# Optimization experiments

Measured on AMD Instinct MI355X. Metric: run time of the kernel, lower is better.

## Reference

```python
import jax, jax.numpy as jnp
import numpy as np

N = 50000      # nodes
E = 800000     # original edges (no self loops)
D = 128        # in_channels == hidden_channels
NEG = 0.2      # leaky_relu negative slope
LAMB = 0.1


def setup_inputs() -> dict:
    key = jax.random.key(0)
    ks = jax.random.split(key, 10)
    s = 0.05
    x = jax.random.normal(ks[0], (N, D), jnp.float32)
    src = jax.random.randint(ks[1], (E,), 0, N)
    off = jax.random.randint(ks[2], (E,), 1, N)
    dst = (src + off) % N  # guaranteed non-self-loop
    loop = jnp.arange(N)
    # add_remaining_self_loops appends the N self loops at the end
    edge_index = jnp.stack([jnp.concatenate([src, loop]),
                            jnp.concatenate([dst, loop])]).astype(jnp.int32)
    return {
        "x": x,
        "edge_index": edge_index,
        "W_gcn": jax.random.normal(ks[3], (D, D), jnp.float32) * s,
        "b_gcn": jnp.zeros((D,), jnp.float32),
        "W_key": jax.random.normal(ks[4], (D, 1), jnp.float32) * s,
        "b_key": jnp.zeros((1,), jnp.float32),
        "W_query": jax.random.normal(ks[5], (D, 1), jnp.float32) * s,
        "b_query": jnp.zeros((1,), jnp.float32),
        "W_rel": jax.random.normal(ks[6], (D, 1), jnp.float32) * s,
        "b_rel": jnp.zeros((1,), jnp.float32),
        "W_root": jax.random.normal(ks[7], (D, 1), jnp.float32) * s,
    }


def _segment_softmax(s, idx, n):
    # numerically stable softmax grouped by idx (every segment nonempty: self loops)
    m = jax.ops.segment_max(s, idx, num_segments=n)
    e = jnp.exp(s - m[idx])
    z = jax.ops.segment_sum(e, idx, num_segments=n)
    return e / z[idx]


def reference(x, edge_index, W_gcn, b_gcn, W_key, b_key, W_query, b_query,
              W_rel, b_rel, W_root):
    n = x.shape[0]
    row, col = edge_index[0], edge_index[1]  # source, target

    # --- GCNConv transform_neighbor (self loops already present) ---
    ew = jnp.ones(row.shape, x.dtype)
    deg = jax.ops.segment_sum(ew, col, num_segments=n)
    dinv = jnp.where(deg > 0, jax.lax.rsqrt(deg), 0.0)
    norm = dinv[row] * dinv[col]                      # [Etot]
    xw = x @ W_gcn                                    # [N, D]
    x_transform = jax.ops.segment_sum(norm[:, None] * xw[row], col,
                                      num_segments=n) + b_gcn  # [N, D]

    x_neighbor = x_transform[col]                     # [Etot, D]

    # key branch: linear -> leaky_relu -> segment softmax over row -> scatter add
    key_s = jax.nn.leaky_relu((x_neighbor @ W_key + b_key)[:, 0], NEG)
    key_s = _segment_softmax(key_s, row, n)[:, None]
    x_reweight_key = jax.ops.segment_sum(x_neighbor * key_s, row, num_segments=n)

    # query branch
    qry_s = jax.nn.leaky_relu((x_neighbor @ W_query + b_query)[:, 0], NEG)
    qry_s = _segment_softmax(qry_s, row, n)[:, None]
    x_reweight_query = jax.ops.segment_sum(x_neighbor * qry_s, row, num_segments=n)

    ker_error = jnp.sum(jnp.abs(x_reweight_key[row] - x_transform[row]), axis=1)
    query_error = jnp.sum(jnp.abs(x_reweight_query[row] - x_transform[col]), axis=1)
    red_score = (ker_error - query_error).at[-n:].set(0.0)  # zero self-loop edges
    score_sum = jax.ops.segment_sum(red_score, row, num_segments=n)

    # --- GraphConv gnn_score: lin_rel(sum_j x_j) + lin_root(x), then sigmoid ---
    agg = jax.ops.segment_sum(x[row], col, num_segments=n)
    fitness = jax.nn.sigmoid((agg @ W_rel + b_rel + x @ W_root)[:, 0])

    return fitness - LAMB * score_sum
```

## Files before the change

### kernel.cpp

```cpp
#include <hip/hip_runtime.h>
#include <math.h>

#define D 128
#define CAP 64
#define NEG 0.2f
#define LAMB 0.1f
#define PB 512
#define SCAP 416
#define NB2 98

__device__ inline float waveReduceSum(float v) {
    #pragma unroll
    for (int m = 32; m; m >>= 1) v += __shfl_xor(v, m);
    return v;
}
__device__ inline float waveReduceMax(float v) {
    #pragma unroll
    for (int m = 32; m; m >>= 1) v = fmaxf(v, __shfl_xor(v, m));
    return v;
}
__device__ inline float blockReduceSum128(float v, float* lds) {
    v = waveReduceSum(v);
    int w = threadIdx.x >> 6;
    if ((threadIdx.x & 63) == 0) lds[w] = v;
    __syncthreads();
    float r = lds[0] + lds[1];
    __syncthreads();
    return r;
}

__device__ inline float bf2f(unsigned short u) {
    union { unsigned int i; float f; } v;
    v.i = ((unsigned int)u) << 16;
    return v.f;
}
__device__ inline float bfLo(unsigned int u) {
    union { unsigned int i; float f; } v;
    v.i = u << 16;
    return v.f;
}
__device__ inline float bfHi(unsigned int u) {
    union { unsigned int i; float f; } v;
    v.i = u & 0xffff0000u;
    return v.f;
}
__device__ inline unsigned short f2bf(float f) {
    union { float f; unsigned int i; } v;
    v.f = f;
    unsigned int b = v.i;
    b += 0x7fff + ((b >> 16) & 1);
    return (unsigned short)(b >> 16);
}

__global__ __launch_bounds__(256) void k_part(
    const int* __restrict__ ei, int etot, int eorig, int q,
    unsigned int* __restrict__ recs, unsigned short* __restrict__ scnt) {
    __shared__ unsigned int bins[16][SCAP];
    __shared__ int bcnt[16];
    const int b = blockIdx.x;
    const int tid = threadIdx.x;
    if (tid < 16) bcnt[tid] = 0;
    __syncthreads();
    const int e0 = (int)((long long)b * eorig / PB);
    const int e1 = (int)((long long)(b + 1) * eorig / PB);
    for (int e = e0 + tid; e < e1; e += 256) {
        int r = ei[e];
        int c = ei[etot + e];
        int gc = c / q;
        int s1 = atomicAdd(&bcnt[gc], 1);
        if (s1 < SCAP) bins[gc][s1] = ((unsigned int)c << 16) | (unsigned int)r;
        int gr = 8 + r / q;
        int s2 = atomicAdd(&bcnt[gr], 1);
        if (s2 < SCAP) bins[gr][s2] = ((unsigned int)r << 16) | (unsigned int)c;
    }
    __syncthreads();
    for (int bk = 0; bk < 16; bk++) {
        int m = min(bcnt[bk], SCAP);
        unsigned int* dst = recs + ((size_t)bk * PB + b) * SCAP;
        for (int i = tid; i < m; i += 256) dst[i] = bins[bk][i];
        if (tid == 0) scnt[bk * PB + b] = (unsigned short)m;
    }
}

__global__ __launch_bounds__(256) void k_partB(
    const unsigned int* __restrict__ recs,
    const unsigned short* __restrict__ scnt, int q,
    unsigned int* __restrict__ recs2, unsigned short* __restrict__ scnt2) {
    const int dirg = blockIdx.x >> 6;
    const int chunk = blockIdx.x & 63;
    const int lo = (dirg & 7) * q;
    __shared__ unsigned int bins[100][64];
    __shared__ int bcnt[100];
    __shared__ int mseg[8];
    const int tid = threadIdx.x;
    for (int i = tid; i < 100; i += 256) bcnt[i] = 0;
    if (tid < 8) mseg[tid] = scnt[dirg * PB + chunk * 8 + tid];
    __syncthreads();
    for (int i = tid; i < 8 * SCAP; i += 256) {
        int seg = i / SCAP, off = i - seg * SCAP;
        if (off < mseg[seg]) {
            unsigned int rec =
                recs[((size_t)dirg * PB + chunk * 8 + seg) * SCAP + off];
            int bk = (int)((rec >> 16) - lo) >> 6;
            if (bk < 100) {
                int s = atomicAdd(&bcnt[bk], 1);
                if (s < 64) bins[bk][s] = rec;
            }
        }
    }
    __syncthreads();
    for (int i = tid; i < NB2 * 64; i += 256) {
        int bk = i >> 6, slot = i & 63;
        int m = min(bcnt[bk], 64);
        if (slot < m)
            recs2[(((size_t)dirg * NB2 + bk) * 64 + chunk) * 64 + slot] =
                bins[bk][slot];
        if (slot == 0)
            scnt2[((size_t)dirg * NB2 + bk) * 64 + chunk] = (unsigned short)m;
    }
}

__global__ __launch_bounds__(256) void k_bld(
    const unsigned int* __restrict__ recs2,
    const unsigned short* __restrict__ scnt2, int q, int n,
    int* __restrict__ cnt_col, int* __restrict__ cnt_row,
    unsigned short* __restrict__ lst_col,
    unsigned short* __restrict__ lst_row) {
    const int dirg = blockIdx.x / NB2;
    const int bk = blockIdx.x - dirg * NB2;
    const int g = dirg & 7;
    const int dir = dirg >> 3;
    const int base = g * q + bk * 64;
    const int hi = min(n, g * q + q);
    const int nb64 = min(64, hi - base);
    if (nb64 <= 0) return;
    __shared__ unsigned short stage[64][CAP];
    __shared__ int scnt3[64];
    __shared__ int mseg[64];
    const int tid = threadIdx.x;
    if (tid < 64) {
        scnt3[tid] = 1;
        stage[tid][0] = (unsigned short)(base + tid);
        mseg[tid] = scnt2[((size_t)dirg * NB2 + bk) * 64 + tid];
    }
    __syncthreads();
    for (int i = tid; i < 64 * 64; i += 256) {
        int seg = i >> 6, slot = i & 63;
        if (slot < mseg[seg]) {
            unsigned int rec =
                recs2[(((size_t)dirg * NB2 + bk) * 64 + seg) * 64 + slot];
            int local = (int)(rec >> 16) - base;
            int s = atomicAdd(&scnt3[local], 1);
            if (s < CAP) stage[local][s] = (unsigned short)(rec & 0xffffu);
        }
    }
    __syncthreads();
    int* cnt = dir ? cnt_row : cnt_col;
    unsigned short* lst = dir ? lst_row : lst_col;
    const int lane = tid & 63;
    const int jo = tid >> 6;
    for (int j0 = 0; j0 < 64; j0 += 4) {
        int j = j0 + jo;
        if (j < nb64) {
            int dg = min(scnt3[j], CAP);
            if (lane < dg) lst[(size_t)(base + j) * CAP + lane] = stage[j][lane];
            if (lane == 0) cnt[base + j] = scnt3[j];
        }
    }
}

__global__ __launch_bounds__(128) void k_gemm(
    const float* __restrict__ x, const float* __restrict__ W,
    const float* __restrict__ Wrel, const float* __restrict__ Wroot,
    unsigned short* __restrict__ xwb, float* __restrict__ xr_rel,
    float* __restrict__ xroot, int n) {
    __shared__ float xs[16][D];
    const int nb = blockIdx.x * 16;
    const int tid = threadIdx.x;
    #pragma unroll
    for (int k = 0; k < 16; k++) {
        int i = nb + k;
        xs[k][tid] = (i < n) ? x[(size_t)i * D + tid] : 0.f;
    }
    __syncthreads();
    float acc[16];
    #pragma unroll
    for (int k = 0; k < 16; k++) acc[k] = 0.f;
    #pragma unroll 4
    for (int d = 0; d < D; d++) {
        float w = W[d * D + tid];
        #pragma unroll
        for (int k = 0; k < 16; k++) acc[k] += xs[k][d] * w;
    }
    #pragma unroll
    for (int k = 0; k < 16; k++) {
        int i = nb + k;
        if (i < n) xwb[(size_t)i * D + tid] = f2bf(acc[k]);
    }
    const int j = tid >> 3;
    const int s = tid & 7;
    float pr = 0.f, po = 0.f;
    #pragma unroll
    for (int e = 0; e < 16; e++) {
        float xv = xs[j][s * 16 + e];
        pr += xv * Wrel[s * 16 + e];
        po += xv * Wroot[s * 16 + e];
    }
    #pragma unroll
    for (int m = 1; m < 8; m <<= 1) {
        pr += __shfl_xor(pr, m);
        po += __shfl_xor(po, m);
    }
    if (s == 0 && nb + j < n) { xr_rel[nb + j] = pr; xroot[nb + j] = po; }
}

__global__ void k_pack(const int* __restrict__ cnt_col,
                       const float* __restrict__ xr_rel,
                       float2* __restrict__ nd, int n) {
    int i = blockIdx.x * blockDim.x + threadIdx.x;
    if (i < n) nd[i] = make_float2(rsqrtf((float)cnt_col[i]), xr_rel[i]);
}

__global__ __launch_bounds__(128) void k_xt(
    const unsigned short* __restrict__ xwb,
    const int* __restrict__ cnt_col, const unsigned short* __restrict__ lst_col,
    const float2* __restrict__ nd, const float* __restrict__ b_gcn,
    const float* __restrict__ Wkey, const float* __restrict__ bkey,
    const float* __restrict__ Wq, const float* __restrict__ bq,
    float* __restrict__ agg_s, unsigned short* __restrict__ xtb,
    float2* __restrict__ lkq, int n) {
    const int c = blockIdx.x;
    const int tid = threadIdx.x;
    const int g = tid >> 5;
    const int l = tid & 31;
    __shared__ int rs[CAP];
    __shared__ float ns[CAP];
    __shared__ float axr[CAP];
    __shared__ float part[4][D];
    __shared__ float red[2];
    int deg = min(cnt_col[c], CAP);
    float dc = nd[c].x;
    if (tid < deg) {
        int rr = lst_col[(size_t)c * CAP + tid];
        rs[tid] = rr;
        float2 t = nd[rr];
        ns[tid] = t.x * dc;
        axr[tid] = t.y;
    }
    __syncthreads();
    if (tid < 64) {
        float av = (tid < deg) ? axr[tid] : 0.f;
        av = waveReduceSum(av);
        if (tid == 0) agg_s[c] = av;
    }
    float4 acc = make_float4(0.f, 0.f, 0.f, 0.f);
#define XSLOT(kk) do {                                                        \
        int k = g + (kk) * 4;                                                 \
        if (k < deg) {                                                        \
            const ushort4 u =                                                 \
                *(const ushort4*)(xwb + (size_t)rs[k] * D + l * 4);           \
            float w = ns[k];                                                  \
            acc.x += w * bf2f(u.x); acc.y += w * bf2f(u.y);                   \
            acc.z += w * bf2f(u.z); acc.w += w * bf2f(u.w);                   \
        }                                                                     \
    } while (0)
    XSLOT(0); XSLOT(1); XSLOT(2); XSLOT(3);
    if (deg > 16) { XSLOT(4); XSLOT(5); }
    if (deg > 24) { XSLOT(6); XSLOT(7); }
    for (int k = g + 32; k < deg; k += 4) {
        const ushort4 u = *(const ushort4*)(xwb + (size_t)rs[k] * D + l * 4);
        float w = ns[k];
        acc.x += w * bf2f(u.x); acc.y += w * bf2f(u.y);
        acc.z += w * bf2f(u.z); acc.w += w * bf2f(u.w);
    }
    *(float4*)(&part[g][l * 4]) = acc;
    __syncthreads();
    float fin = part[0][tid] + part[1][tid] + part[2][tid] + part[3][tid]
                + b_gcn[tid];
    xtb[(size_t)c * D + tid] = f2bf(fin);
    float sk = blockReduceSum128(fin * Wkey[tid], red);
    float sq = blockReduceSum128(fin * Wq[tid], red);
    if (tid == 0) {
        float vk = sk + bkey[0];
        float vq = sq + bq[0];
        lkq[c] = make_float2(vk > 0.f ? vk : NEG * vk,
                             vq > 0.f ? vq : NEG * vq);
    }
}

__global__ __launch_bounds__(128) void k_fused(
    const unsigned short* __restrict__ xtb,
    const int* __restrict__ cnt_row, const unsigned short* __restrict__ lst_row,
    const float2* __restrict__ lkq,
    const float* __restrict__ agg_s, const float* __restrict__ xroot,
    const float* __restrict__ brel, float* __restrict__ out, int n) {
    const int r = blockIdx.x;
    const int tid = threadIdx.x;
    const int g = tid >> 5;
    const int l = tid & 31;
    __shared__ int cs[CAP];
    __shared__ float al[CAP], be[CAP];
    __shared__ float p1[4][D], p2[4][D];
    __shared__ float xrq_row[D];
    __shared__ float red[2];
    int deg = min(cnt_row[r], CAP);
    float xtr = bf2f(xtb[(size_t)r * D + tid]);
    if (tid < deg) {
        int c = lst_row[(size_t)r * CAP + tid];
        cs[tid] = c;
        float2 t = lkq[c];
        al[tid] = t.x;
        be[tid] = t.y;
    }
    __syncthreads();
    uint2 vr[8];
#define LSLOT(kk) do {                                                        \
        int k_ = g + (kk) * 4;                                                \
        vr[kk] = make_uint2(0u, 0u);                                          \
        if (k_ < deg)                                                         \
            vr[kk] = *(const uint2*)(xtb + (size_t)cs[k_] * D + l * 4);       \
    } while (0)
    LSLOT(0); LSLOT(1); LSLOT(2); LSLOT(3);
    if (deg > 16) { LSLOT(4); LSLOT(5); }
    if (deg > 24) { LSLOT(6); LSLOT(7); }
    if (tid < 64) {
        float vk = (tid < deg) ? al[tid] : -3.4e38f;
        float vq = (tid < deg) ? be[tid] : -3.4e38f;
        float mk = waveReduceMax(vk);
        float mq = waveReduceMax(vq);
        float ek = (tid < deg) ? __expf(al[tid] - mk) : 0.f;
        float eq = (tid < deg) ? __expf(be[tid] - mq) : 0.f;
        float zk = waveReduceSum(ek);
        float zq = waveReduceSum(eq);
        if (tid < deg) { al[tid] = ek / zk; be[tid] = eq / zq; }
    }
    __syncthreads();
    float4 xrk = make_float4(0.f, 0.f, 0.f, 0.f);
    float4 xrq = make_float4(0.f, 0.f, 0.f, 0.f);
#define GSLOT(kk) do {                                                        \
        int k_ = g + (kk) * 4;                                                \
        float a_ = 0.f, b_ = 0.f;                                             \
        if (k_ < deg) { a_ = al[k_]; b_ = be[k_]; }                           \
        float v0 = bfLo(vr[kk].x), v1 = bfHi(vr[kk].x);                       \
        float v2 = bfLo(vr[kk].y), v3 = bfHi(vr[kk].y);                       \
        xrk.x += a_ * v0; xrk.y += a_ * v1;                                   \
        xrk.z += a_ * v2; xrk.w += a_ * v3;                                   \
        xrq.x += b_ * v0; xrq.y += b_ * v1;                                   \
        xrq.z += b_ * v2; xrq.w += b_ * v3;                                   \
    } while (0)
    GSLOT(0); GSLOT(1); GSLOT(2); GSLOT(3);
    if (deg > 16) { GSLOT(4); GSLOT(5); }
    if (deg > 24) { GSLOT(6); GSLOT(7); }
    for (int k = g + 32; k < deg; k += 4) {
        const ushort4 u = *(const ushort4*)(xtb + (size_t)cs[k] * D + l * 4);
        float a = al[k], b = be[k];
        xrk.x += a * bf2f(u.x); xrk.y += a * bf2f(u.y);
        xrk.z += a * bf2f(u.z); xrk.w += a * bf2f(u.w);
        xrq.x += b * bf2f(u.x); xrq.y += b * bf2f(u.y);
        xrq.z += b * bf2f(u.z); xrq.w += b * bf2f(u.w);
    }
    *(float4*)(&p1[g][l * 4]) = xrk;
    *(float4*)(&p2[g][l * 4]) = xrq;
    __syncthreads();
    float xrk_c = p1[0][tid] + p1[1][tid] + p1[2][tid] + p1[3][tid];
    float xrq_c = p2[0][tid] + p2[1][tid] + p2[2][tid] + p2[3][tid];
    xrq_row[tid] = xrq_c;
    float KE = blockReduceSum128(fabsf(xrk_c - xtr), red);
    const float4 q4 = *(const float4*)(&xrq_row[l * 4]);
    float sp = 0.f;
#define QSLOT(kk) do {                                                        \
        int k_ = g + (kk) * 4;                                                \
        if (k_ < deg && cs[k_] != r) {                                        \
            sp += fabsf(q4.x - bfLo(vr[kk].x)) + fabsf(q4.y - bfHi(vr[kk].x)) \
                + fabsf(q4.z - bfLo(vr[kk].y)) + fabsf(q4.w - bfHi(vr[kk].y));\
        }                                                                     \
    } while (0)
    QSLOT(0); QSLOT(1); QSLOT(2); QSLOT(3);
    if (deg > 16) { QSLOT(4); QSLOT(5); }
    if (deg > 24) { QSLOT(6); QSLOT(7); }
    for (int k = g + 32; k < deg; k += 4) {
        if (cs[k] != r) {
            const ushort4 u = *(const ushort4*)(xtb + (size_t)cs[k] * D + l * 4);
            sp += fabsf(q4.x - bf2f(u.x)) + fabsf(q4.y - bf2f(u.y)) +
                  fabsf(q4.z - bf2f(u.z)) + fabsf(q4.w - bf2f(u.w));
        }
    }
    float SQE = blockReduceSum128(sp, red);
    if (tid == 0) {
        float score = (float)(deg - 1) * KE - SQE;
        float z = agg_s[r] + brel[0] + xroot[r];
        float f = 1.f / (1.f + __expf(-z));
        out[r] = f - LAMB * score;
    }
}

extern "C" void kernel_launch(void* const* d_in, const int* in_sizes, int n_in,
                              void* d_out, int out_size, void* d_ws, size_t ws_size,
                              hipStream_t stream) {
    const float* x    = (const float*)d_in[0];
    const int*   ei   = (const int*)d_in[1];
    const float* Wg   = (const float*)d_in[2];
    const float* bg   = (const float*)d_in[3];
    const float* Wk   = (const float*)d_in[4];
    const float* bk   = (const float*)d_in[5];
    const float* Wq   = (const float*)d_in[6];
    const float* bq   = (const float*)d_in[7];
    const float* Wr   = (const float*)d_in[8];
    const float* br   = (const float*)d_in[9];
    const float* Wo   = (const float*)d_in[10];

    const int n = in_sizes[0] / D;
    const int etot = in_sizes[1] / 2;
    const int eorig = etot - n;
    const int q = (n + 7) / 8;

    char* ws = (char*)d_ws;
    size_t off = 0;
    auto alloc = [&](size_t bytes) -> void* {
        void* p = ws + off;
        off += (bytes + 255) & ~(size_t)255;
        return p;
    };
    unsigned short* xwb = (unsigned short*)alloc((size_t)n * D * 2);
    unsigned short* xtb = (unsigned short*)alloc((size_t)n * D * 2);
    size_t recsA_bytes = (size_t)16 * PB * SCAP * 4;
    size_t lst_bytes   = (size_t)n * CAP * 2 * 2;
    char* unionA = (char*)alloc(recsA_bytes > lst_bytes ? recsA_bytes
                                                        : lst_bytes);
    unsigned int*   recsA   = (unsigned int*)unionA;
    unsigned short* lst_col = (unsigned short*)unionA;
    unsigned short* lst_row = (unsigned short*)(unionA + (size_t)n * CAP * 2);
    unsigned int*   recs2 = (unsigned int*)alloc((size_t)16 * NB2 * 64 * 64 * 4);
    unsigned short* scnt  = (unsigned short*)alloc((size_t)16 * PB * 2);
    unsigned short* scnt2 = (unsigned short*)alloc((size_t)16 * NB2 * 64 * 2);
    int*    cnt_col = (int*)alloc((size_t)n * 4);
    int*    cnt_row = (int*)alloc((size_t)n * 4);
    float*  agg_s   = (float*)alloc((size_t)n * 4);
    float2* lkq     = (float2*)alloc((size_t)n * 8);
    float2* nd      = (float2*)alloc((size_t)n * 8);
    float*  xr_rel  = (float*)alloc((size_t)n * 4);
    float*  xroot   = (float*)alloc((size_t)n * 4);

    k_part<<<PB, 256, 0, stream>>>(ei, etot, eorig, q, recsA, scnt);
    k_partB<<<16 * 64, 256, 0, stream>>>(recsA, scnt, q, recs2, scnt2);
    k_bld<<<16 * NB2, 256, 0, stream>>>(recs2, scnt2, q, n,
                                        cnt_col, cnt_row, lst_col, lst_row);
    k_gemm<<<(n + 15) / 16, 128, 0, stream>>>(x, Wg, Wr, Wo, xwb, xr_rel,
                                              xroot, n);
    k_pack<<<(n + 255) / 256, 256, 0, stream>>>(cnt_col, xr_rel, nd, n);
    k_xt<<<n, 128, 0, stream>>>(xwb, cnt_col, lst_col, nd, bg, Wk, bk,
                                Wq, bq, agg_s, xtb, lkq, n);
    k_fused<<<n, 128, 0, stream>>>(xtb, cnt_row, lst_row, lkq,
                                   agg_s, xroot, br, (float*)d_out, n);
}
```

Before: 196.6 us.

## Compute GCN weight GEMM with bf16 MFMA instead of scalar FMA loops

Replaces the scalar fp32 x@W_gcn loop with bf16 MFMA 16x16x32 instructions. A new tiny kernel transposes W into bf16 first, and each block now handles 32 rows staged as bf16 in LDS. Results go back through LDS for coalesced 16-byte stores. This cuts the ALU cost of the dense transform, but the input is now rounded to bf16 before multiplying, and the xr_rel/xroot dot products also read the bf16 copy, which loses precision.

```diff
diff --git a/kernel.cpp b/kernel.cpp
--- a/kernel.cpp
+++ b/kernel.cpp
@@ -8,6 +8,10 @@
 #define PB 512
 #define SCAP 416
 #define NB2 98
+#define XS 136
+
+typedef __attribute__((ext_vector_type(8))) short bf16x8;
+typedef __attribute__((ext_vector_type(4))) float f32x4;
 
 __device__ inline float waveReduceSum(float v) {
     #pragma unroll
@@ -169,49 +173,79 @@
     }
 }
 
+__global__ __launch_bounds__(128) void k_wt(const float* __restrict__ W,
+                                            unsigned short* __restrict__ Wt) {
+    int idx = blockIdx.x * 128 + threadIdx.x;
+    int col = idx >> 7, k = idx & 127;
+    Wt[col * 128 + k] = f2bf(W[k * 128 + col]);
+}
+
 __global__ __launch_bounds__(128) void k_gemm(
-    const float* __restrict__ x, const float* __restrict__ W,
+    const float* __restrict__ x, const unsigned short* __restrict__ Wt,
     const float* __restrict__ Wrel, const float* __restrict__ Wroot,
     unsigned short* __restrict__ xwb, float* __restrict__ xr_rel,
     float* __restrict__ xroot, int n) {
-    __shared__ float xs[16][D];
-    const int nb = blockIdx.x * 16;
-    const int tid = threadIdx.x;
-    #pragma unroll
-    for (int k = 0; k < 16; k++) {
-        int i = nb + k;
-        xs[k][tid] = (i < n) ? x[(size_t)i * D + tid] : 0.f;
-    }
-    __syncthreads();
-    float acc[16];
-    #pragma unroll
-    for (int k = 0; k < 16; k++) acc[k] = 0.f;
-    #pragma unroll 4
-    for (int d = 0; d < D; d++) {
-        float w = W[d * D + tid];
+    __shared__ unsigned short xbf[32][XS];
+    const int tid = threadIdx.x;
+    const int nb = blockIdx.x * 32;
+    for (int idx = tid; idx < 32 * 128; idx += 128) {
+        int row = idx >> 7, col = idx & 127;
+        int i = nb + row;
+        xbf[row][col] = (i < n) ? f2bf(x[(size_t)i * D + col]) : 0;
+    }
+    __syncthreads();
+    {
+        const int j = tid >> 2;
+        const int s = tid & 3;
+        float pr = 0.f, po = 0.f;
         #pragma unroll
-        for (int k = 0; k < 16; k++) acc[k] += xs[k][d] * w;
-    }
-    #pragma unroll
-    for (int k = 0; k < 16; k++) {
-        int i = nb + k;
-        if (i < n) xwb[(size_t)i * D + tid] = f2bf(acc[k]);
-    }
-    const int j = tid >> 3;
-    const int s = tid & 7;
-    float pr = 0.f, po = 0.f;
-    #pragma unroll
-    for (int e = 0; e < 16; e++) {
-        float xv = xs[j][s * 16 + e];
-        pr += xv * Wrel[s * 16 + e];
-        po += xv * Wroot[s * 16 + e];
-    }
-    #pragma unroll
-    for (int m = 1; m < 8; m <<= 1) {
-        pr += __shfl_xor(pr, m);
-        po += __shfl_xor(po, m);
-    }
-    if (s == 0 && nb + j < n) { xr_rel[nb + j] = pr; xroot[nb + j] = po; }
+        for (int e = 0; e < 32; e++) {
+            float xv = bf2f(xbf[j][s * 32 + e]);
+            pr += xv * Wrel[s * 32 + e];
+            po += xv * Wroot[s * 32 + e];
+        }
+        pr += __shfl_xor(pr, 1); po += __shfl_xor(po, 1);
+        pr += __shfl_xor(pr, 2); po += __shfl_xor(po, 2);
+        if (s == 0 && nb + j < n) { xr_rel[nb + j] = pr; xroot[nb + j] = po; }
+    }
+    const int w = tid >> 6;
+    const int l = tid & 63;
+    const int row16 = l & 15;
+    const int kb = (l >> 4) * 8;
+    bf16x8 afr[4];
+    #pragma unroll
+    for (int t = 0; t < 4; t++)
+        afr[t] = *(const bf16x8*)&xbf[w * 16 + row16][t * 32 + kb];
+    __syncthreads();
+    f32x4 acc[8];
+    #pragma unroll
+    for (int nt = 0; nt < 8; nt++) acc[nt] = (f32x4){0.f, 0.f, 0.f, 0.f};
+    #pragma unroll
+    for (int t = 0; t < 4; t++) {
+        #pragma unroll
+        for (int nt = 0; nt < 8; nt++) {
+            bf16x8 bfr = *(const bf16x8*)
+                &Wt[(size_t)(nt * 16 + row16) * 128 + t * 32 + kb];
+            acc[nt] = __builtin_amdgcn_mfma_f32_16x16x32_bf16(
+                afr[t], bfr, acc[nt], 0, 0, 0);
+        }
+    }
+    #pragma unroll
+    for (int nt = 0; nt < 8; nt++) {
+        #pragma unroll
+        for (int rr = 0; rr < 4; rr++) {
+            int row = w * 16 + (l >> 4) * 4 + rr;
+            xbf[row][nt * 16 + row16] = f2bf(acc[nt][rr]);
+        }
+    }
+    __syncthreads();
+    for (int idx = tid; idx < 32 * 16; idx += 128) {
+        int row = idx >> 4, chunk = idx & 15;
+        int i = nb + row;
+        if (i < n)
+            *(uint4*)&xwb[(size_t)i * D + chunk * 8] =
+                *(const uint4*)&xbf[row][chunk * 8];
+    }
 }
 
 __global__ void k_pack(const int* __restrict__ cnt_col,
@@ -440,12 +474,14 @@
     float2* nd      = (float2*)alloc((size_t)n * 8);
     float*  xr_rel  = (float*)alloc((size_t)n * 4);
     float*  xroot   = (float*)alloc((size_t)n * 4);
+    unsigned short* Wt = (unsigned short*)alloc((size_t)128 * 128 * 2);
 
     k_part<<<PB, 256, 0, stream>>>(ei, etot, eorig, q, recsA, scnt);
     k_partB<<<16 * 64, 256, 0, stream>>>(recsA, scnt, q, recs2, scnt2);
     k_bld<<<16 * NB2, 256, 0, stream>>>(recs2, scnt2, q, n,
                                         cnt_col, cnt_row, lst_col, lst_row);
-    k_gemm<<<(n + 15) / 16, 128, 0, stream>>>(x, Wg, Wr, Wo, xwb, xr_rel,
+    k_wt<<<128, 128, 0, stream>>>(Wg, Wt);
+    k_gemm<<<(n + 31) / 32, 128, 0, stream>>>(x, Wt, Wr, Wo, xwb, xr_rel,
                                               xroot, n);
     k_pack<<<(n + 255) / 256, 256, 0, stream>>>(cnt_col, xr_rel, nd, n);
     k_xt<<<n, 128, 0, stream>>>(xwb, cnt_col, lst_col, nd, bg, Wk, bk,
```

Result: faster. 186.8 us (-5.0%).
